# Kernel tuning notes

Measured on AMD Instinct MI355X. Metric: run time of the kernel, lower is better.

## Reference

```python
import jax, jax.numpy as jnp
import numpy as np

B, T, H, W, C = 32, 32, 28, 28, 1
F = 48   # conv filters
U = 8    # lstm units
EPS = 1e-3  # keras BatchNormalization default epsilon


def setup_inputs() -> dict:
    key = jax.random.key(0)
    ks = jax.random.split(key, 10)
    s = lambda fan_in: 1.0 / np.sqrt(fan_in)
    return {
        "x": jax.random.normal(ks[0], (B, T, H, W, C), jnp.float32),
        "w1": jax.random.normal(ks[1], (3, 3, C, F), jnp.float32) * s(9 * C),
        "b1": jnp.zeros((F,), jnp.float32),
        "w2": jax.random.normal(ks[2], (3, 3, F, F), jnp.float32) * s(9 * F),
        "b2": jnp.zeros((F,), jnp.float32),
        "w3": jax.random.normal(ks[3], (3, 3, F, F), jnp.float32) * s(9 * F),
        "b3": jnp.zeros((F,), jnp.float32),
        "bn1_g": jnp.ones((F,), jnp.float32),
        "bn1_b": jnp.zeros((F,), jnp.float32),
        "bn1_m": jnp.zeros((F,), jnp.float32),
        "bn1_v": jnp.ones((F,), jnp.float32),
        "wf": jax.random.normal(ks[4], (F + U, U), jnp.float32) * s(F + U),
        "bf": jnp.zeros((U,), jnp.float32),
        "wi1": jax.random.normal(ks[5], (F + U, U), jnp.float32) * s(F + U),
        "bi1": jnp.zeros((U,), jnp.float32),
        "wi2": jax.random.normal(ks[6], (F + U, U), jnp.float32) * s(F + U),
        "bi2": jnp.zeros((U,), jnp.float32),
        "wo": jax.random.normal(ks[7], (F + U, U), jnp.float32) * s(F + U),
        "bo": jnp.zeros((U,), jnp.float32),
        "bn2_g": jnp.ones((U,), jnp.float32),
        "bn2_b": jnp.zeros((U,), jnp.float32),
        "bn2_m": jnp.zeros((U,), jnp.float32),
        "bn2_v": jnp.ones((U,), jnp.float32),
        "w_out": jax.random.normal(ks[8], (U, 1), jnp.float32) * s(U),
        "b_out": jnp.zeros((1,), jnp.float32),
    }


def _conv_relu(x, w, b):
    # x: [N, H, W, Cin], w: [3, 3, Cin, Cout], SAME padding
    y = jax.lax.conv_general_dilated(
        x, w, window_strides=(1, 1), padding="SAME",
        dimension_numbers=("NHWC", "HWIO", "NHWC"))
    return jax.nn.relu(y + b)


def _bn_inf(x, g, b, m, v):
    return (x - m) * jax.lax.rsqrt(v + EPS) * g + b


def _forward(x, w1, b1, w2, b2, w3, b3, bn1_g, bn1_b, bn1_m, bn1_v,
             wf, bf, wi1, bi1, wi2, bi2, wo, bo,
             bn2_g, bn2_b, bn2_m, bn2_v, w_out, b_out):
    Bb, Tt = x.shape[0], x.shape[1]
    xf = x.reshape(Bb * Tt, H, W, C)            # fold time into batch for convs
    xf = _conv_relu(xf, w1, b1)
    xf = _conv_relu(xf, w2, b2)
    xf = _conv_relu(xf, w3, b3)
    xf = _bn_inf(xf, bn1_g, bn1_b, bn1_m, bn1_v)
    feats = xf.mean(axis=(1, 2)).reshape(Bb, Tt, F)   # GlobalAvgPool2D per frame

    def step(carry, xt):
        c, h = carry
        z = jnp.concatenate([xt, h], axis=-1)          # [B, F+U]
        f = jax.nn.sigmoid(z @ wf + bf)
        i = jax.nn.sigmoid(z @ wi1 + bi1)
        g = jnp.tanh(z @ wi2 + bi2)
        o = jax.nn.sigmoid(z @ wo + bo)
        c_new = f * c + i * g
        h_new = o * jnp.tanh(c_new)
        return (c_new, h_new), h_new

    init = (jnp.zeros((Bb, U), x.dtype), jnp.zeros((Bb, U), x.dtype))
    _, hs = jax.lax.scan(step, init, jnp.swapaxes(feats, 0, 1))  # [T, B, U]
    hs = jnp.swapaxes(hs, 0, 1)                                   # [B, T, U]
    y = _bn_inf(hs, bn2_g, bn2_b, bn2_m, bn2_v)
    return y @ w_out + b_out                                      # [B, T, 1]


def reference(x, w1, b1, w2, b2, w3, b3, bn1_g, bn1_b, bn1_m, bn1_v,
              wf, bf, wi1, bi1, wi2, bi2, wo, bo,
              bn2_g, bn2_b, bn2_m, bn2_v, w_out, b_out):
    return _forward(x, w1, b1, w2, b2, w3, b3, bn1_g, bn1_b, bn1_m, bn1_v,
                    wf, bf, wi1, bi1, wi2, bi2, wo, bo,
                    bn2_g, bn2_b, bn2_m, bn2_v, w_out, b_out)
```

## Files before the change

### kernel.cpp

```cpp
#include <hip/hip_runtime.h>
#include <stdint.h>

#define B_ 32
#define T_ 32
#define NPIX 784
#define NFRM 1024
#define EPSV 1e-3f

typedef __attribute__((ext_vector_type(8))) _Float16 half8v;
typedef __attribute__((ext_vector_type(4))) float float4v;

#define W_BYTES  43008
#define X_OFF    43008
#define ACT_OFF  46144
#define CB_STRIDE 12576
#define ZERO_OFF (ACT_OFF + 6 * CB_STRIDE)
#define LDS_TOT  (ZERO_OFF + 16)

__device__ __forceinline__ unsigned short f2h(float f) {
    union { _Float16 h; unsigned short u; } cv; cv.h = (_Float16)f; return cv.u;
}

__global__ __launch_bounds__(256) void pack_weights(
    const float* __restrict__ w2, const float* __restrict__ w3,
    unsigned short* __restrict__ out)
{
    int idx = blockIdx.x * 256 + threadIdx.x;
    int conv = idx / 21504;
    int r = idx - conv * 21504;
    const float* w = conv ? w3 : w2;
    int s  = r / 1536;
    int r2 = r - s * 1536;
    int q  = r2 / 384;
    int r3 = r2 - q * 384;
    int co = r3 >> 3, j = r3 & 7;
    int k  = s * 32 + q * 8 + j;
    unsigned short v = 0;
    if (k < 432) v = f2h(w[k * 48 + co]);
    out[idx] = v;
}

__device__ __forceinline__ void stage_w(char* smem, const char* g, int tid) {
    int lane = tid & 63, wid = tid >> 6;
    const char* gl = g + lane * 16;
    for (int c = wid; c < 42; c += 8) {
        int off = c * 1024;
        __builtin_amdgcn_global_load_lds(
            (const __attribute__((address_space(1))) unsigned int*)(gl + off),
            (__attribute__((address_space(3))) unsigned int*)(smem + off),
            16, 0, 0);
    }
}

#define KLOOP                                                                  \
    _Pragma("unroll")                                                          \
    for (int s = 0; s < 14; ++s) {                                             \
        const char* wb = smem + bB + s * 3072;                                 \
        half8v bv0 = *(const half8v*)(wb);                                     \
        half8v bv1 = *(const half8v*)(wb + 256);                               \
        half8v bv2 = *(const half8v*)(wb + 512);                               \
        _Pragma("unroll")                                                      \
        for (int mt = 0; mt < 7; ++mt) {                                       \
            int ad = pixb16[mt] + aoff_s[s];                                   \
            ad = ((msk[mt] >> tap_s[s]) & 1) ? ad : ZERO_OFF;                  \
            half8v a = *(const half8v*)(smem + ad);                            \
            acc[mt][0] = __builtin_amdgcn_mfma_f32_16x16x32_f16(a, bv0, acc[mt][0], 0, 0, 0); \
            acc[mt][1] = __builtin_amdgcn_mfma_f32_16x16x32_f16(a, bv1, acc[mt][1], 0, 0, 0); \
            acc[mt][2] = __builtin_amdgcn_mfma_f32_16x16x32_f16(a, bv2, acc[mt][2], 0, 0, 0); \
        }                                                                      \
    }

__global__ __launch_bounds__(512, 1) void fused_cnn(
    const float* __restrict__ x,
    const float* __restrict__ w1, const float* __restrict__ b1,
    const float* __restrict__ b2, const float* __restrict__ b3,
    const unsigned short* __restrict__ wpack,
    float* __restrict__ feats,
    const float* __restrict__ bn_g, const float* __restrict__ bn_b,
    const float* __restrict__ bn_m, const float* __restrict__ bn_v)
{
    __shared__ __align__(16) char smem[LDS_TOT];
    const int tid = threadIdx.x;
    const int n = blockIdx.x;
    const int lane = tid & 63, wid = tid >> 6;
    const int l15 = lane & 15, q = lane >> 4;

    if (tid < 4) *(unsigned int*)(smem + ZERO_OFF + tid * 4) = 0;
    stage_w(smem, (const char*)wpack, tid);
    {
        const float* xf = x + (size_t)n * NPIX;
        float* sx = (float*)(smem + X_OFF);
        for (int i = tid; i < NPIX; i += 512) sx[i] = xf[i];
    }
    __syncthreads();

    {
        const float* sx = (const float*)(smem + X_OFF);
        for (int rnd = 0; rnd < 2; ++rnd) {
            int p = tid + rnd * 512;
            if (p < NPIX) {
                int y = p / 28, xx = p % 28;
                float a[48];
                #pragma unroll
                for (int c = 0; c < 48; ++c) a[c] = b1[c];
                #pragma unroll
                for (int dy = 0; dy < 3; ++dy) {
                    int yy = y + dy - 1;
                    if ((unsigned)yy >= 28u) continue;
                    #pragma unroll
                    for (int dx = 0; dx < 3; ++dx) {
                        int xc = xx + dx - 1;
                        if ((unsigned)xc >= 28u) continue;
                        float xv = sx[yy * 28 + xc];
                        const float* wr = w1 + (dy * 3 + dx) * 48;
                        #pragma unroll
                        for (int c = 0; c < 48; ++c) a[c] += xv * wr[c];
                    }
                }
                #pragma unroll
                for (int cb = 0; cb < 6; ++cb) {
                    half8v h;
                    #pragma unroll
                    for (int j = 0; j < 8; ++j)
                        h[j] = (_Float16)fmaxf(a[cb * 8 + j], 0.f);
                    *(half8v*)(smem + ACT_OFF + cb * CB_STRIDE + p * 16) = h;
                }
            }
        }
    }
    __syncthreads();

    int tap_s[14], aoff_s[14];
    #pragma unroll
    for (int s = 0; s < 14; ++s) {
        int k = s * 32 + q * 8;
        int tap = k / 48;
        int kc  = k - tap * 48;
        int ty = tap / 3, tx = tap - ty * 3;
        tap_s[s]  = tap;
        aoff_s[s] = ACT_OFF + (kc >> 3) * CB_STRIDE + (ty * 28 + tx) * 16;
    }
    const int bB = q * 768 + l15 * 16;
    float bias2[3], bias3[3];
    #pragma unroll
    for (int nt = 0; nt < 3; ++nt) {
        bias2[nt] = b2[nt * 16 + l15];
        bias3[nt] = b3[nt * 16 + l15];
    }

    float4v acc[7][3];
    int pixb16[7], msk[7];
    #pragma unroll
    for (int mt = 0; mt < 7; ++mt) {
        int tt = wid + mt * 8;
        int p  = tt * 16 + l15;
        int y  = (p * 9363) >> 18;
        int x2 = p - y * 28;
        pixb16[mt] = (p - 29) * 16;
        unsigned my0 = ((unsigned)(y - 1) < 28u) ? 0x007u : 0u;
        unsigned my1 = ((unsigned)(y    ) < 28u) ? 0x038u : 0u;
        unsigned my2 = ((unsigned)(y + 1) < 28u) ? 0x1C0u : 0u;
        unsigned mx0 = ((unsigned)(x2 - 1) < 28u) ? 0x049u : 0u;
        unsigned mx1 = ((unsigned)(x2    ) < 28u) ? 0x092u : 0u;
        unsigned mx2 = ((unsigned)(x2 + 1) < 28u) ? 0x124u : 0u;
        msk[mt] = (int)((my0 | my1 | my2) & (mx0 | mx1 | mx2));
        if (tt >= 49) msk[mt] = 0;
        #pragma unroll
        for (int nt = 0; nt < 3; ++nt)
            acc[mt][nt] = (float4v){bias2[nt], bias2[nt], bias2[nt], bias2[nt]};
    }

    KLOOP

    __syncthreads();
    stage_w(smem, (const char*)wpack + W_BYTES, tid);

    #pragma unroll
    for (int mt = 0; mt < 7; ++mt) {
        int tt = wid + mt * 8;
        if (tt >= 49) continue;
        #pragma unroll
        for (int nt = 0; nt < 3; ++nt) {
            int c = nt * 16 + l15;
            char* base = smem + ACT_OFF + (c >> 3) * CB_STRIDE + (c & 7) * 2;
            #pragma unroll
            for (int r = 0; r < 4; ++r) {
                int p = tt * 16 + q * 4 + r;
                *(unsigned short*)(base + p * 16) = f2h(fmaxf(acc[mt][nt][r], 0.f));
            }
        }
    }
    __syncthreads();

    #pragma unroll
    for (int mt = 0; mt < 7; ++mt)
        #pragma unroll
        for (int nt = 0; nt < 3; ++nt)
            acc[mt][nt] = (float4v){bias3[nt], bias3[nt], bias3[nt], bias3[nt]};

    KLOOP

    float ps0 = 0.f, ps1 = 0.f, ps2 = 0.f;
    #pragma unroll
    for (int mt = 0; mt < 7; ++mt) {
        int tt = wid + mt * 8;
        if (tt >= 49) continue;
        #pragma unroll
        for (int r = 0; r < 4; ++r) {
            ps0 += fmaxf(acc[mt][0][r], 0.f);
            ps1 += fmaxf(acc[mt][1][r], 0.f);
            ps2 += fmaxf(acc[mt][2][r], 0.f);
        }
    }
    ps0 += __shfl_xor(ps0, 16); ps0 += __shfl_xor(ps0, 32);
    ps1 += __shfl_xor(ps1, 16); ps1 += __shfl_xor(ps1, 32);
    ps2 += __shfl_xor(ps2, 16); ps2 += __shfl_xor(ps2, 32);
    __syncthreads();
    float* sRed = (float*)smem;
    if (lane < 16) {
        sRed[wid * 48 + l15]      = ps0;
        sRed[wid * 48 + 16 + l15] = ps1;
        sRed[wid * 48 + 32 + l15] = ps2;
    }
    __syncthreads();
    if (tid < 48) {
        float s = 0.f;
        #pragma unroll
        for (int wv = 0; wv < 8; ++wv) s += sRed[wv * 48 + tid];
        float r  = rsqrtf(bn_v[tid] + EPSV);
        float sc = r * bn_g[tid] * (1.0f / 784.0f);
        float sh = bn_b[tid] - bn_m[tid] * r * bn_g[tid];
        feats[(size_t)n * 48 + tid] = s * sc + sh;
    }
}

__global__ __launch_bounds__(64) void lstm_kernel(
    const float* __restrict__ feats,
    const float* __restrict__ wf, const float* __restrict__ bfv,
    const float* __restrict__ wi1, const float* __restrict__ bi1,
    const float* __restrict__ wi2, const float* __restrict__ bi2,
    const float* __restrict__ wo, const float* __restrict__ bov,
    const float* __restrict__ g2, const float* __restrict__ b2v,
    const float* __restrict__ m2, const float* __restrict__ v2,
    const float* __restrict__ w_out, const float* __restrict__ b_out,
    float* __restrict__ out)
{
    __shared__ float sW[4][56][8];
    __shared__ float sBias[4][8];
    __shared__ float sZ[64];
    __shared__ float sGate[4][8];
    __shared__ float sH[8];
    __shared__ float sS[8];
    __shared__ float sK;

    int tid = threadIdx.x;
    int b = blockIdx.x;

    for (int i = tid; i < 56 * 8; i += 64) {
        (&sW[0][0][0])[i] = wf[i];
        (&sW[1][0][0])[i] = wi1[i];
        (&sW[2][0][0])[i] = wi2[i];
        (&sW[3][0][0])[i] = wo[i];
    }
    if (tid < 8) {
        sBias[0][tid] = bfv[tid];  sBias[1][tid] = bi1[tid];
        sBias[2][tid] = bi2[tid];  sBias[3][tid] = bov[tid];
        float r = rsqrtf(v2[tid] + EPSV);
        sS[tid] = r * g2[tid] * w_out[tid];
        sH[tid] = 0.0f;
    }
    if (tid == 0) {
        float k = b_out[0];
        for (int u = 0; u < 8; u++) {
            float r = rsqrtf(v2[u] + EPSV);
            k += (b2v[u] - m2[u] * r * g2[u]) * w_out[u];
        }
        sK = k;
    }
    __syncthreads();

    float c = 0.0f;
    const float* fb = feats + (size_t)b * T_ * 48;

    for (int t = 0; t < T_; t++) {
        if (tid < 48) sZ[tid] = fb[t * 48 + tid];
        else if (tid < 56) sZ[tid] = sH[tid - 48];
        __syncthreads();

        if (tid < 32) {
            int g = tid >> 3, u = tid & 7;
            float a = sBias[g][u];
            #pragma unroll
            for (int k = 0; k < 56; k++) a += sZ[k] * sW[g][k][u];
            float v = (g == 2) ? tanhf(a) : 1.0f / (1.0f + __expf(-a));
            sGate[g][u] = v;
        }
        __syncthreads();

        if (tid < 8) {
            c = sGate[0][tid] * c + sGate[1][tid] * sGate[2][tid];
            float h = sGate[3][tid] * tanhf(c);
            sH[tid] = h;
            float contrib = h * sS[tid];
            contrib += __shfl_xor(contrib, 1);
            contrib += __shfl_xor(contrib, 2);
            contrib += __shfl_xor(contrib, 4);
            if (tid == 0) out[b * T_ + t] = contrib + sK;
        }
        __syncthreads();
    }
}

extern "C" void kernel_launch(void* const* d_in, const int* in_sizes, int n_in,
                              void* d_out, int out_size, void* d_ws, size_t ws_size,
                              hipStream_t stream)
{
    const float* x    = (const float*)d_in[0];
    const float* w1   = (const float*)d_in[1];
    const float* b1   = (const float*)d_in[2];
    const float* w2   = (const float*)d_in[3];
    const float* b2   = (const float*)d_in[4];
    const float* w3   = (const float*)d_in[5];
    const float* b3   = (const float*)d_in[6];
    const float* bn1g = (const float*)d_in[7];
    const float* bn1b = (const float*)d_in[8];
    const float* bn1m = (const float*)d_in[9];
    const float* bn1v = (const float*)d_in[10];
    const float* wf   = (const float*)d_in[11];
    const float* bf   = (const float*)d_in[12];
    const float* wi1  = (const float*)d_in[13];
    const float* bi1  = (const float*)d_in[14];
    const float* wi2  = (const float*)d_in[15];
    const float* bi2  = (const float*)d_in[16];
    const float* wo   = (const float*)d_in[17];
    const float* bo   = (const float*)d_in[18];
    const float* bn2g = (const float*)d_in[19];
    const float* bn2b = (const float*)d_in[20];
    const float* bn2m = (const float*)d_in[21];
    const float* bn2v = (const float*)d_in[22];
    const float* wout = (const float*)d_in[23];
    const float* bout = (const float*)d_in[24];

    unsigned short* wpack = (unsigned short*)d_ws;
    float* feats = (float*)((char*)d_ws + 2 * W_BYTES);
    const size_t need = 2 * W_BYTES + (size_t)NFRM * 48 * 4;
    if (ws_size < need) return;

    pack_weights<<<168, 256, 0, stream>>>(w2, w3, wpack);
    fused_cnn<<<NFRM, 512, 0, stream>>>(x, w1, b1, b2, b3, wpack, feats,
                                        bn1g, bn1b, bn1m, bn1v);
    lstm_kernel<<<B_, 64, 0, stream>>>(feats, wf, bf, wi1, bi1, wi2, bi2, wo, bo,
                                       bn2g, bn2b, bn2m, bn2v, wout, bout,
                                       (float*)d_out);
}
```

Before: 126.0 us.

## Stream conv weights from global/L2 to shrink LDS and raise occupancy; register-resident LSTM

Packed conv2/conv3 weights are no longer staged into LDS. Each wave now reads its B fragments directly from global memory (L2-cached), which cuts LDS use from about 120KB to about 78KB so that more than one 512-thread block can fit per CU. The launch bound is raised to 4 waves per SIMD and the padded 7th m-tile is skipped for all waves except wave 0. The LSTM kernel keeps its gate weights in registers, splits the 56-long dot product across two half-waves joined by a shuffle, and replaces tanhf with exp-based formulas. The cost is global-load latency inside the MFMA inner loop and higher register pressure from the tighter launch bound.

```diff
diff --git a/kernel.cpp b/kernel.cpp
--- a/kernel.cpp
+++ b/kernel.cpp
@@ -10,12 +10,11 @@
 typedef __attribute__((ext_vector_type(8))) _Float16 half8v;
 typedef __attribute__((ext_vector_type(4))) float float4v;
 
-#define W_BYTES  43008
-#define X_OFF    43008
-#define ACT_OFF  46144
 #define CB_STRIDE 12576
-#define ZERO_OFF (ACT_OFF + 6 * CB_STRIDE)
-#define LDS_TOT  (ZERO_OFF + 16)
+#define ZERO_OFF  75456
+#define X_OFF     75472
+#define LDS_TOT   78608
+#define WPACK     43008
 
 __device__ __forceinline__ unsigned short f2h(float f) {
     union { _Float16 h; unsigned short u; } cv; cv.h = (_Float16)f; return cv.u;
@@ -40,37 +39,27 @@
     out[idx] = v;
 }
 
-__device__ __forceinline__ void stage_w(char* smem, const char* g, int tid) {
-    int lane = tid & 63, wid = tid >> 6;
-    const char* gl = g + lane * 16;
-    for (int c = wid; c < 42; c += 8) {
-        int off = c * 1024;
-        __builtin_amdgcn_global_load_lds(
-            (const __attribute__((address_space(1))) unsigned int*)(gl + off),
-            (__attribute__((address_space(3))) unsigned int*)(smem + off),
-            16, 0, 0);
-    }
-}
-
-#define KLOOP                                                                  \
+#define KLOOP(GW)                                                              \
     _Pragma("unroll")                                                          \
     for (int s = 0; s < 14; ++s) {                                             \
-        const char* wb = smem + bB + s * 3072;                                 \
+        const char* wb = (GW) + bB + s * 3072;                                 \
         half8v bv0 = *(const half8v*)(wb);                                     \
         half8v bv1 = *(const half8v*)(wb + 256);                               \
         half8v bv2 = *(const half8v*)(wb + 512);                               \
         _Pragma("unroll")                                                      \
         for (int mt = 0; mt < 7; ++mt) {                                       \
-            int ad = pixb16[mt] + aoff_s[s];                                   \
-            ad = ((msk[mt] >> tap_s[s]) & 1) ? ad : ZERO_OFF;                  \
-            half8v a = *(const half8v*)(smem + ad);                            \
-            acc[mt][0] = __builtin_amdgcn_mfma_f32_16x16x32_f16(a, bv0, acc[mt][0], 0, 0, 0); \
-            acc[mt][1] = __builtin_amdgcn_mfma_f32_16x16x32_f16(a, bv1, acc[mt][1], 0, 0, 0); \
-            acc[mt][2] = __builtin_amdgcn_mfma_f32_16x16x32_f16(a, bv2, acc[mt][2], 0, 0, 0); \
+            if (mt < 6 || wid == 0) {                                          \
+                int ad = pixb16[mt] + aoff_s[s];                               \
+                ad = ((msk[mt] >> tap_s[s]) & 1) ? ad : ZERO_OFF;              \
+                half8v a = *(const half8v*)(smem + ad);                        \
+                acc[mt][0] = __builtin_amdgcn_mfma_f32_16x16x32_f16(a, bv0, acc[mt][0], 0, 0, 0); \
+                acc[mt][1] = __builtin_amdgcn_mfma_f32_16x16x32_f16(a, bv1, acc[mt][1], 0, 0, 0); \
+                acc[mt][2] = __builtin_amdgcn_mfma_f32_16x16x32_f16(a, bv2, acc[mt][2], 0, 0, 0); \
+            }                                                                  \
         }                                                                      \
     }
 
-__global__ __launch_bounds__(512, 1) void fused_cnn(
+__global__ __launch_bounds__(512, 4) void fused_cnn(
     const float* __restrict__ x,
     const float* __restrict__ w1, const float* __restrict__ b1,
     const float* __restrict__ b2, const float* __restrict__ b3,
@@ -86,7 +75,6 @@
     const int l15 = lane & 15, q = lane >> 4;
 
     if (tid < 4) *(unsigned int*)(smem + ZERO_OFF + tid * 4) = 0;
-    stage_w(smem, (const char*)wpack, tid);
     {
         const float* xf = x + (size_t)n * NPIX;
         float* sx = (float*)(smem + X_OFF);
@@ -123,7 +111,7 @@
                     #pragma unroll
                     for (int j = 0; j < 8; ++j)
                         h[j] = (_Float16)fmaxf(a[cb * 8 + j], 0.f);
-                    *(half8v*)(smem + ACT_OFF + cb * CB_STRIDE + p * 16) = h;
+                    *(half8v*)(smem + cb * CB_STRIDE + p * 16) = h;
                 }
             }
         }
@@ -138,9 +126,11 @@
         int kc  = k - tap * 48;
         int ty = tap / 3, tx = tap - ty * 3;
         tap_s[s]  = tap;
-        aoff_s[s] = ACT_OFF + (kc >> 3) * CB_STRIDE + (ty * 28 + tx) * 16;
+        aoff_s[s] = (kc >> 3) * CB_STRIDE + (ty * 28 + tx) * 16;
     }
     const int bB = q * 768 + l15 * 16;
+    const char* gw2 = (const char*)wpack;
+    const char* gw3 = gw2 + WPACK;
     float bias2[3], bias3[3];
     #pragma unroll
     for (int nt = 0; nt < 3; ++nt) {
@@ -170,10 +160,9 @@
             acc[mt][nt] = (float4v){bias2[nt], bias2[nt], bias2[nt], bias2[nt]};
     }
 
-    KLOOP
-
-    __syncthreads();
-    stage_w(smem, (const char*)wpack + W_BYTES, tid);
+    KLOOP(gw2)
+
+    __syncthreads();
 
     #pragma unroll
     for (int mt = 0; mt < 7; ++mt) {
@@ -182,7 +171,7 @@
         #pragma unroll
         for (int nt = 0; nt < 3; ++nt) {
             int c = nt * 16 + l15;
-            char* base = smem + ACT_OFF + (c >> 3) * CB_STRIDE + (c & 7) * 2;
+            char* base = smem + (c >> 3) * CB_STRIDE + (c & 7) * 2;
             #pragma unroll
             for (int r = 0; r < 4; ++r) {
                 int p = tt * 16 + q * 4 + r;
@@ -198,7 +187,7 @@
         for (int nt = 0; nt < 3; ++nt)
             acc[mt][nt] = (float4v){bias3[nt], bias3[nt], bias3[nt], bias3[nt]};
 
-    KLOOP
+    KLOOP(gw3)
 
     float ps0 = 0.f, ps1 = 0.f, ps2 = 0.f;
     #pragma unroll
@@ -245,67 +234,63 @@
     const float* __restrict__ w_out, const float* __restrict__ b_out,
     float* __restrict__ out)
 {
-    __shared__ float sW[4][56][8];
-    __shared__ float sBias[4][8];
-    __shared__ float sZ[64];
-    __shared__ float sGate[4][8];
-    __shared__ float sH[8];
+    __shared__ float sZ[56];
+    __shared__ float sG[32];
     __shared__ float sS[8];
-    __shared__ float sK;
+    __shared__ float sKs;
 
     int tid = threadIdx.x;
     int b = blockIdx.x;
-
-    for (int i = tid; i < 56 * 8; i += 64) {
-        (&sW[0][0][0])[i] = wf[i];
-        (&sW[1][0][0])[i] = wi1[i];
-        (&sW[2][0][0])[i] = wi2[i];
-        (&sW[3][0][0])[i] = wo[i];
-    }
+    int gu = tid & 31, g = gu >> 3, u = gu & 7, half = tid >> 5;
+
+    const float* wsrc = (g == 0) ? wf : (g == 1) ? wi1 : (g == 2) ? wi2 : wo;
+    float wreg[28];
+    #pragma unroll
+    for (int j = 0; j < 28; ++j) wreg[j] = wsrc[(half * 28 + j) * 8 + u];
+    float bias = ((g == 0) ? bfv : (g == 1) ? bi1 : (g == 2) ? bi2 : bov)[u];
+
     if (tid < 8) {
-        sBias[0][tid] = bfv[tid];  sBias[1][tid] = bi1[tid];
-        sBias[2][tid] = bi2[tid];  sBias[3][tid] = bov[tid];
         float r = rsqrtf(v2[tid] + EPSV);
         sS[tid] = r * g2[tid] * w_out[tid];
-        sH[tid] = 0.0f;
+        sZ[48 + tid] = 0.f;
     }
     if (tid == 0) {
         float k = b_out[0];
-        for (int u = 0; u < 8; u++) {
-            float r = rsqrtf(v2[u] + EPSV);
-            k += (b2v[u] - m2[u] * r * g2[u]) * w_out[u];
-        }
-        sK = k;
-    }
-    __syncthreads();
-
-    float c = 0.0f;
+        for (int uu = 0; uu < 8; ++uu) {
+            float r = rsqrtf(v2[uu] + EPSV);
+            k += (b2v[uu] - m2[uu] * r * g2[uu]) * w_out[uu];
+        }
+        sKs = k;
+    }
+
+    float c = 0.f;
     const float* fb = feats + (size_t)b * T_ * 48;
 
-    for (int t = 0; t < T_; t++) {
+    for (int t = 0; t < T_; ++t) {
         if (tid < 48) sZ[tid] = fb[t * 48 + tid];
-        else if (tid < 56) sZ[tid] = sH[tid - 48];
         __syncthreads();
 
-        if (tid < 32) {
-            int g = tid >> 3, u = tid & 7;
-            float a = sBias[g][u];
-            #pragma unroll
-            for (int k = 0; k < 56; k++) a += sZ[k] * sW[g][k][u];
-            float v = (g == 2) ? tanhf(a) : 1.0f / (1.0f + __expf(-a));
-            sGate[g][u] = v;
-        }
+        float a = 0.f;
+        #pragma unroll
+        for (int j = 0; j < 28; ++j) a += sZ[half * 28 + j] * wreg[j];
+        a += __shfl_xor(a, 32);
+        a += bias;
+        float v;
+        if (g == 2) { float e = __expf(2.f * a); v = 1.f - 2.f / (e + 1.f); }
+        else        { v = 1.f / (1.f + __expf(-a)); }
+        if (tid < 32) sG[gu] = v;
         __syncthreads();
 
         if (tid < 8) {
-            c = sGate[0][tid] * c + sGate[1][tid] * sGate[2][tid];
-            float h = sGate[3][tid] * tanhf(c);
-            sH[tid] = h;
+            c = sG[tid] * c + sG[8 + tid] * sG[16 + tid];
+            float e = __expf(2.f * c);
+            float h = sG[24 + tid] * (1.f - 2.f / (e + 1.f));
+            sZ[48 + tid] = h;
             float contrib = h * sS[tid];
             contrib += __shfl_xor(contrib, 1);
             contrib += __shfl_xor(contrib, 2);
             contrib += __shfl_xor(contrib, 4);
-            if (tid == 0) out[b * T_ + t] = contrib + sK;
+            if (tid == 0) out[b * T_ + t] = contrib + sKs;
         }
         __syncthreads();
     }
@@ -342,8 +327,8 @@
     const float* bout = (const float*)d_in[24];
 
     unsigned short* wpack = (unsigned short*)d_ws;
-    float* feats = (float*)((char*)d_ws + 2 * W_BYTES);
-    const size_t need = 2 * W_BYTES + (size_t)NFRM * 48 * 4;
+    float* feats = (float*)((char*)d_ws + 2 * WPACK);
+    const size_t need = 2 * WPACK + (size_t)NFRM * 48 * 4;
     if (ws_size < need) return;
 
     pack_weights<<<168, 256, 0, stream>>>(w2, w3, wpack);
```

Result: slower. 241.5 us (+91.7%).
